# Optimization experiments

Hardware: AMD Instinct MI355X
Metric: run time of the kernel (lower is better)

The kernel has to match this reference:

```python
import jax, jax.numpy as jnp
import numpy as np

N = 100000
HEADS = 8
HID = 8  # per-head channels of gat1
NUM_CLASSES = 40
NUM_FEATURES = 256
NEG_SLOPE = 0.2


def gat_conv(x, src, dst, W, att_src, att_dst, bias, heads, out_ch, concat):
    # x: [N, F_in]; src/dst: [E] (self-loops already included)
    n = x.shape[0]
    h = (x @ W).reshape(n, heads, out_ch)                      # [N, H, C]
    a_src = jnp.sum(h * att_src, axis=-1)                      # [N, H]
    a_dst = jnp.sum(h * att_dst, axis=-1)                      # [N, H]
    e = jax.nn.leaky_relu(a_src[src] + a_dst[dst], NEG_SLOPE)  # [E, H]
    # segment softmax over edges grouped by destination node
    e_max = jax.ops.segment_max(e, dst, num_segments=n)        # [N, H]
    w = jnp.exp(e - e_max[dst])                                # [E, H]
    denom = jax.ops.segment_sum(w, dst, num_segments=n)        # [N, H]
    alpha = w / (denom[dst] + 1e-16)                           # [E, H]
    out = jax.ops.segment_sum(h[src] * alpha[:, :, None], dst, num_segments=n)  # [N, H, C]
    out = out.reshape(n, heads * out_ch) if concat else out.mean(axis=1)
    return out + bias


def setup_inputs() -> dict:
    key = jax.random.key(0)
    ks = jax.random.split(key, 12)
    x = jax.random.normal(ks[0], (N, NUM_FEATURES), dtype=jnp.float32)
    edge_index = jax.random.randint(ks[1], (2, 3200000), 0, N, dtype=jnp.int64)
    g1 = (2.0 / (NUM_FEATURES + HEADS * HID)) ** 0.5
    g2 = (2.0 / (HEADS * HID + NUM_CLASSES)) ** 0.5
    return {
        "x": x,
        "edge_index": edge_index,
        "W1": jax.random.normal(ks[2], (NUM_FEATURES, HEADS * HID), dtype=jnp.float32) * g1,
        "att_src1": jax.random.normal(ks[3], (HEADS, HID), dtype=jnp.float32) * g1,
        "att_dst1": jax.random.normal(ks[4], (HEADS, HID), dtype=jnp.float32) * g1,
        "b1": jnp.zeros((HEADS * HID,), dtype=jnp.float32),
        "W2": jax.random.normal(ks[5], (HEADS * HID, NUM_CLASSES), dtype=jnp.float32) * g2,
        "att_src2": jax.random.normal(ks[6], (1, NUM_CLASSES), dtype=jnp.float32) * g2,
        "att_dst2": jax.random.normal(ks[7], (1, NUM_CLASSES), dtype=jnp.float32) * g2,
        "b2": jnp.zeros((NUM_CLASSES,), dtype=jnp.float32),
    }


def reference(x, edge_index, W1, att_src1, att_dst1, b1, W2, att_src2, att_dst2, b2):
    n = x.shape[0]
    # add self loops (PyG GATConv default) -> every segment is non-empty
    loops = jnp.arange(n, dtype=edge_index.dtype)
    src = jnp.concatenate([edge_index[0], loops])
    dst = jnp.concatenate([edge_index[1], loops])
    # dropout is identity in eval mode
    h = gat_conv(x, src, dst, W1, att_src1, att_dst1, b1, HEADS, HID, concat=True)
    h = jax.nn.elu(h)
    out = gat_conv(h, src, dst, W2, att_src2, att_dst2, b2, 1, NUM_CLASSES, concat=False)
    return jax.nn.log_softmax(out, axis=1)
```

## Files before the change

### kernel.cpp

```cpp
#include <hip/hip_runtime.h>
#include <hip/hip_bf16.h>
#include <cstdint>
#include <cstddef>

#define NNODES 100000
#define NEDGES 3200000
#define NTOT   3300000
#define FIN    256
#define HH     64
#define NH     8
#define C2     40
#define NEG    0.2f

#define CHUNK  8192
#define NBLK   403
#define NBKT   391

typedef __hip_bfloat16 bf16;
typedef __attribute__((ext_vector_type(8))) short short8;
typedef __attribute__((ext_vector_type(4))) float f32x4;


__global__ __launch_bounds__(256) void k_bhist(const int* __restrict__ ei, int* __restrict__ bhist) {
    __shared__ int h[NBKT];
    int t = threadIdx.x;
    for (int b = t; b < NBKT; b += 256) h[b] = 0;
    __syncthreads();
    int i0 = blockIdx.x * CHUNK;
    int i1 = i0 + CHUNK; if (i1 > NTOT) i1 = NTOT;
    for (int i = i0 + t; i < i1; i += 256) {
        int d = (i < NEDGES) ? ei[NEDGES + i] : (i - NEDGES);
        atomicAdd(&h[d >> 8], 1);
    }
    __syncthreads();
    for (int b = t; b < NBKT; b += 256) bhist[b * NBLK + blockIdx.x] = h[b];
}

__global__ __launch_bounds__(512) void k_bscan(int* __restrict__ bhist, int* __restrict__ bktTot) {
    __shared__ int sm[512];
    int t = threadIdx.x, b = blockIdx.x;
    int v = (t < NBLK) ? bhist[b * NBLK + t] : 0;
    sm[t] = v;
    __syncthreads();
    for (int off = 1; off < 512; off <<= 1) {
        int u = (t >= off) ? sm[t - off] : 0;
        __syncthreads();
        sm[t] += u;
        __syncthreads();
    }
    if (t < NBLK) bhist[b * NBLK + t] = sm[t] - v;
    if (t == NBLK - 1) bktTot[b] = sm[t];
}

__global__ __launch_bounds__(512) void k_base(const int* __restrict__ bktTot, int* __restrict__ bktBase,
                                              int* __restrict__ rowptr) {
    __shared__ int sm[512];
    int t = threadIdx.x;
    int v = (t < NBKT) ? bktTot[t] : 0;
    sm[t] = v;
    __syncthreads();
    for (int off = 1; off < 512; off <<= 1) {
        int u = (t >= off) ? sm[t - off] : 0;
        __syncthreads();
        sm[t] += u;
        __syncthreads();
    }
    if (t < NBKT) bktBase[t] = sm[t] - v;
    if (t == NBKT - 1) bktBase[NBKT] = sm[t];
    if (t == 0) rowptr[NNODES] = NTOT;
}

__global__ __launch_bounds__(256) void k_scat1(const int* __restrict__ ei, const int* __restrict__ bhist,
                                               const int* __restrict__ bktBase, unsigned int* __restrict__ pb) {
    __shared__ int cur[NBKT];
    int t = threadIdx.x, blk = blockIdx.x;
    for (int b = t; b < NBKT; b += 256) cur[b] = bktBase[b] + bhist[b * NBLK + blk];
    __syncthreads();
    int i0 = blk * CHUNK;
    int i1 = i0 + CHUNK; if (i1 > NTOT) i1 = NTOT;
    for (int i = i0 + t; i < i1; i += 256) {
        int s, d;
        if (i < NEDGES) { s = ei[i]; d = ei[NEDGES + i]; }
        else            { s = d = i - NEDGES; }
        int p = atomicAdd(&cur[d >> 8], 1);
        pb[p] = ((unsigned)s << 8) | (unsigned)(d & 255);
    }
}

__global__ __launch_bounds__(256) void k_bucket(const unsigned int* __restrict__ pb,
                                                const int* __restrict__ bktBase,
                                                int* __restrict__ rowptr, int* __restrict__ esrc) {
    __shared__ int dcnt[256];
    __shared__ int sm[256];
    __shared__ int cur[256];
    int t = threadIdx.x, b = blockIdx.x;
    int base = bktBase[b], cnt = bktBase[b + 1] - base;
    dcnt[t] = 0;
    __syncthreads();
    for (int i = t; i < cnt; i += 256) atomicAdd(&dcnt[pb[base + i] & 255], 1);
    __syncthreads();
    int v = dcnt[t];
    sm[t] = v;
    __syncthreads();
    for (int off = 1; off < 256; off <<= 1) {
        int u = (t >= off) ? sm[t - off] : 0;
        __syncthreads();
        sm[t] += u;
        __syncthreads();
    }
    int ex = sm[t] - v;
    int n = (b << 8) + t;
    if (n < NNODES) rowptr[n] = base + ex;
    cur[t] = base + ex;
    __syncthreads();
    for (int i = t; i < cnt; i += 256) {
        unsigned int e = pb[base + i];
        int p = atomicAdd(&cur[e & 255], 1);
        esrc[p] = (int)(e >> 8);
    }
}


__global__ __launch_bounds__(256) void k_wcvt(const float* __restrict__ W, bf16* __restrict__ Wf) {
    int idx = blockIdx.x * 256 + threadIdx.x;
    int j = idx & 7, slot = idx >> 3;
    int l = slot & 63, sf = slot >> 6;
    int s = sf >> 2, f = sf & 3;
    int k = s * 32 + (l >> 4) * 8 + j;
    int c = 16 * f + (l & 15);
    Wf[idx] = __float2bfloat16(W[k * HH + c]);
}

__global__ __launch_bounds__(256) void k_gemm1(const float* __restrict__ x, const bf16* __restrict__ Wf,
                                               const float* __restrict__ asw, const float* __restrict__ adw,
                                               bf16* __restrict__ h1b, float* __restrict__ as,
                                               float* __restrict__ ad) {
    __shared__ short xs[64][256];
    int t = threadIdx.x;
    int n0 = blockIdx.x * 64;
    {
        int r = t >> 2, cq = t & 3;
        int n = n0 + r; if (n >= NNODES) n = NNODES - 1;
        const float4* xr = (const float4*)(x + (size_t)n * FIN + cq * 64);
        int sw = r & 7;
#pragma unroll
        for (int u = 0; u < 8; ++u) {
            float4 p0 = xr[2 * u], p1 = xr[2 * u + 1];
            float tmp[8] = {p0.x, p0.y, p0.z, p0.w, p1.x, p1.y, p1.z, p1.w};
            short8 v;
#pragma unroll
            for (int e = 0; e < 8; ++e) {
                bf16 b = __float2bfloat16(tmp[e]);
                v[e] = *reinterpret_cast<short*>(&b);
            }
            int kb = cq * 8 + u;
            *(short8*)&xs[r][(kb ^ sw) << 3] = v;
        }
    }
    __syncthreads();
    int l = t & 63, wv = t >> 6;
    int rbase = wv * 16;
    int lr = l & 15, g = l >> 4;
    f32x4 acc[4] = {{0.f,0.f,0.f,0.f},{0.f,0.f,0.f,0.f},{0.f,0.f,0.f,0.f},{0.f,0.f,0.f,0.f}};
    const short8* wfp = (const short8*)Wf;
#pragma unroll 2
    for (int s = 0; s < 8; ++s) {
        short8 a = *(const short8*)&xs[rbase + lr][((s * 4 + g) ^ (lr & 7)) << 3];
#pragma unroll
        for (int f = 0; f < 4; ++f) {
            short8 b = wfp[(s * 4 + f) * 64 + l];
            acc[f] = __builtin_amdgcn_mfma_f32_16x16x32_bf16(a, b, acc[f], 0, 0, 0);
        }
    }
    float awf[4], dwf[4];
#pragma unroll
    for (int f = 0; f < 4; ++f) { awf[f] = asw[16 * f + lr]; dwf[f] = adw[16 * f + lr]; }
    float svv[4][4], dvv[4][4];
#pragma unroll
    for (int f = 0; f < 4; ++f) {
#pragma unroll
        for (int j = 0; j < 4; ++j) {
            float val = acc[f][j];
            int n = n0 + rbase + g * 4 + j;
            if (n < NNODES) h1b[(size_t)n * HH + 16 * f + lr] = __float2bfloat16(val);
            float sv = val * awf[f], dv = val * dwf[f];
            sv += __shfl_xor(sv, 1); sv += __shfl_xor(sv, 2); sv += __shfl_xor(sv, 4);
            dv += __shfl_xor(dv, 1); dv += __shfl_xor(dv, 2); dv += __shfl_xor(dv, 4);
            svv[f][j] = sv; dvv[f][j] = dv;
        }
    }
    if ((l & 7) == 0) {
        int hb = (l >> 3) & 1;
#pragma unroll
        for (int f = 0; f < 4; ++f) {
            int h = 2 * f + hb;
#pragma unroll
            for (int j = 0; j < 4; ++j) {
                int n = n0 + rbase + g * 4 + j;
                if (n < NNODES) { as[n * NH + h] = svv[f][j]; ad[n * NH + h] = dvv[f][j]; }
            }
        }
    }
}

__global__ __launch_bounds__(256) void k_aggr1(const bf16* __restrict__ h1b, const float* __restrict__ as,
                                               const float* __restrict__ ad, const int* __restrict__ rowptr,
                                               const int* __restrict__ esrc, const float* __restrict__ b1,
                                               float* __restrict__ hmid) {
    __shared__ float wlds[4][64];
    int wv = threadIdx.x >> 6, t = threadIdx.x & 63;
    int n = blockIdx.x * 4 + wv;
    int ih = t & 7;
    int ie = t >> 3;
    int h  = t >> 3;
    float adh = ad[n * NH + ih];
    int beg = __builtin_amdgcn_readfirstlane(rowptr[n]);
    int end = __builtin_amdgcn_readfirstlane(rowptr[n + 1]);
    float acc = 0.f, den_e = 0.f;
    int idx0 = beg + ie; if (idx0 >= end) idx0 = end - 1;
    int s_t = esrc[idx0];
    float a_t = as[s_t * NH + ih];
    for (int j0 = beg; j0 < end; j0 += 8) {
        int m = end - j0; if (m > 8) m = 8;
        float e = a_t + adh;
        e = (e > 0.f) ? e : NEG * e;
        float w_t = (ie < m) ? __expf(e) : 0.f;
        den_e += w_t;
        wlds[wv][t] = w_t;
        __builtin_amdgcn_wave_barrier();
        if (j0 + 8 < end) {
            int idx = j0 + 8 + ie; if (idx >= end) idx = end - 1;
            s_t = esrc[idx];
            a_t = as[s_t * NH + ih];
        }
        const int* ep = esrc + j0;
        if (m == 8) {
#pragma unroll
            for (int k = 0; k < 8; ++k) {
                int sk = __builtin_amdgcn_readfirstlane(ep[k]);
                float vk = __bfloat162float(h1b[(size_t)sk * HH + t]);
                acc = fmaf(wlds[wv][k * 8 + h], vk, acc);
            }
        } else {
            for (int k = 0; k < m; ++k) {
                int sk = __builtin_amdgcn_readfirstlane(ep[k]);
                float vk = __bfloat162float(h1b[(size_t)sk * HH + t]);
                acc = fmaf(wlds[wv][k * 8 + h], vk, acc);
            }
        }
        __builtin_amdgcn_wave_barrier();
    }
    den_e += __shfl_xor(den_e, 8);
    den_e += __shfl_xor(den_e, 16);
    den_e += __shfl_xor(den_e, 32);
    float den = __shfl(den_e, h);
    float o = acc / (den + 1e-16f) + b1[t];
    hmid[(size_t)n * HH + t] = (o > 0.f) ? o : expm1f(o);
}


__global__ __launch_bounds__(256) void k_gemm2(const float* __restrict__ hmid, const float* __restrict__ W2,
                                               const float* __restrict__ as2w, const float* __restrict__ ad2w,
                                               bf16* __restrict__ h2b, float* __restrict__ as2,
                                               float* __restrict__ ad2) {
    __shared__ float w2s[64 * C2];
    __shared__ float hrow[4][64];
    int t = threadIdx.x;
    for (int i = t; i < 64 * C2; i += 256) w2s[i] = W2[i];
    __syncthreads();
    int wv = t >> 6, ln = t & 63;
    int n = blockIdx.x * 4 + wv;
    hrow[wv][ln] = hmid[(size_t)n * HH + ln];
    __syncthreads();
    float acc = 0.f;
    if (ln < C2) {
#pragma unroll 8
        for (int k = 0; k < 64; ++k) acc = fmaf(hrow[wv][k], w2s[k * C2 + ln], acc);
    }
    float sv = 0.f, dv = 0.f;
    if (ln < C2) {
        h2b[(size_t)n * C2 + ln] = __float2bfloat16(acc);
        sv = acc * as2w[ln];
        dv = acc * ad2w[ln];
    }
#pragma unroll
    for (int off = 32; off > 0; off >>= 1) {
        sv += __shfl_xor(sv, off);
        dv += __shfl_xor(dv, off);
    }
    if (ln == 0) { as2[n] = sv; ad2[n] = dv; }
}

__global__ __launch_bounds__(256) void k_aggr2(const bf16* __restrict__ h2b, const float* __restrict__ as2,
                                               const float* __restrict__ ad2, const int* __restrict__ rowptr,
                                               const int* __restrict__ esrc, const float* __restrict__ b2,
                                               float* __restrict__ out) {
    int wv = threadIdx.x >> 6, t = threadIdx.x & 63;
    int n = blockIdx.x * 4 + wv;
    float adn = ad2[n];
    int beg = __builtin_amdgcn_readfirstlane(rowptr[n]);
    int end = __builtin_amdgcn_readfirstlane(rowptr[n + 1]);
    bool act = (t < C2);
    int tc = act ? t : 0;
    float acc = 0.f, den_p = 0.f;
    for (int j0 = beg; j0 < end; j0 += 64) {
        int m = end - j0; if (m > 64) m = 64;
        int idx = j0 + t; if (idx >= end) idx = end - 1;
        int s_t = esrc[idx];
        float e = as2[s_t] + adn;
        e = (e > 0.f) ? e : NEG * e;
        float w_t = (t < m) ? __expf(e) : 0.f;
        den_p += w_t;
        const int* ep = esrc + j0;
        int k = 0;
        for (; k + 8 <= m; k += 8) {
#pragma unroll
            for (int u = 0; u < 8; ++u) {
                int sk = __builtin_amdgcn_readfirstlane(ep[k + u]);
                float wk = __shfl(w_t, k + u);
                acc = fmaf(wk, __bfloat162float(h2b[(size_t)sk * C2 + tc]), acc);
            }
        }
        for (; k < m; ++k) {
            int sk = __builtin_amdgcn_readfirstlane(ep[k]);
            float wk = __shfl(w_t, k);
            acc = fmaf(wk, __bfloat162float(h2b[(size_t)sk * C2 + tc]), acc);
        }
    }
    float den = den_p;
#pragma unroll
    for (int off = 32; off > 0; off >>= 1) den += __shfl_xor(den, off);
    float o = act ? (acc / (den + 1e-16f) + b2[t]) : -1e30f;
    float mx = o;
#pragma unroll
    for (int off = 32; off > 0; off >>= 1) mx = fmaxf(mx, __shfl_xor(mx, off));
    float ex = act ? __expf(o - mx) : 0.f;
    float sm = ex;
#pragma unroll
    for (int off = 32; off > 0; off >>= 1) sm += __shfl_xor(sm, off);
    if (act) out[(size_t)n * C2 + t] = o - mx - logf(sm);
}


extern "C" void kernel_launch(void* const* d_in, const int* in_sizes, int n_in,
                              void* d_out, int out_size, void* d_ws, size_t ws_size,
                              hipStream_t stream) {
    const float* x    = (const float*)d_in[0];
    const int*   ei   = (const int*)d_in[1];
    const float* W1   = (const float*)d_in[2];
    const float* as1w = (const float*)d_in[3];
    const float* ad1w = (const float*)d_in[4];
    const float* b1   = (const float*)d_in[5];
    const float* W2   = (const float*)d_in[6];
    const float* as2w = (const float*)d_in[7];
    const float* ad2w = (const float*)d_in[8];
    const float* b2   = (const float*)d_in[9];
    float* out = (float*)d_out;

    char* ws = (char*)d_ws;
    bf16*  h1b     = (bf16*) (ws + 0);
    float* as1     = (float*)(ws + 12800000);
    float* ad1     = (float*)(ws + 16000000);
    float* hmid    = (float*)(ws + 19200000);
    unsigned int* pb = (unsigned int*)(ws + 19200000);
    bf16*  h2b     = (bf16*) (ws + 44800000);
    int*   bhist   = (int*)  (ws + 44800000);
    float* as2     = (float*)(ws + 52800000);
    int*   bktBase = (int*)  (ws + 52800000);
    float* ad2     = (float*)(ws + 53200000);
    int*   bktTot  = (int*)  (ws + 53200000);
    int*   rowp    = (int*)  (ws + 53600000);
    int*   esrc    = (int*)  (ws + 54000256);
    bf16*  Wf      = (bf16*) (ws + 67201024);

    k_bhist <<<NBLK, 256, 0, stream>>>(ei, bhist);
    k_bscan <<<NBKT, 512, 0, stream>>>(bhist, bktTot);
    k_base  <<<1,    512, 0, stream>>>(bktTot, bktBase, rowp);
    k_scat1 <<<NBLK, 256, 0, stream>>>(ei, bhist, bktBase, pb);
    k_bucket<<<NBKT, 256, 0, stream>>>(pb, bktBase, rowp, esrc);
    k_wcvt  <<<64, 256, 0, stream>>>(W1, Wf);
    k_gemm1 <<<(NNODES + 63) / 64, 256, 0, stream>>>(x, Wf, as1w, ad1w, h1b, as1, ad1);
    k_aggr1 <<<NNODES / 4, 256, 0, stream>>>(h1b, as1, ad1, rowp, esrc, b1, hmid);
    k_gemm2 <<<NNODES / 4, 256, 0, stream>>>(hmid, W2, as2w, ad2w, h2b, as2, ad2);
    k_aggr2 <<<NNODES / 4, 256, 0, stream>>>(h2b, as2, ad2, rowp, esrc, b2, out);
}
```

Measured before the change: 349.1 us.

## Split layer-1 features into head-pair quarters and aggregate per quarter

Layer-1 features and source attention scores are stored in four head-pair planes, so each plane is a compact 3.2 MB (features) or 0.8 MB (scores) array. The layer-1 aggregation now launches one block per quarter of four nodes, so each gather touches only that quarter's plane. It also processes 64 edges per wave iteration, with 4 edges gathered in parallel across lane groups. This aims to improve cache locality of the random source-node gathers and edge-level parallelism, at the cost of reading the edge list and row pointers four times and more blocks.

```diff
diff --git a/kernel.cpp b/kernel.cpp
--- a/kernel.cpp
+++ b/kernel.cpp
@@ -133,7 +133,7 @@
 
 __global__ __launch_bounds__(256) void k_gemm1(const float* __restrict__ x, const bf16* __restrict__ Wf,
                                                const float* __restrict__ asw, const float* __restrict__ adw,
-                                               bf16* __restrict__ h1b, float* __restrict__ as,
+                                               bf16* __restrict__ h1q, float* __restrict__ as1q,
                                                float* __restrict__ ad) {
     __shared__ short xs[64][256];
     int t = threadIdx.x;
@@ -182,7 +182,7 @@
         for (int j = 0; j < 4; ++j) {
             float val = acc[f][j];
             int n = n0 + rbase + g * 4 + j;
-            if (n < NNODES) h1b[(size_t)n * HH + 16 * f + lr] = __float2bfloat16(val);
+            if (n < NNODES) h1q[(size_t)f * (NNODES * 16) + (size_t)n * 16 + lr] = __float2bfloat16(val);
             float sv = val * awf[f], dv = val * dwf[f];
             sv += __shfl_xor(sv, 1); sv += __shfl_xor(sv, 2); sv += __shfl_xor(sv, 4);
             dv += __shfl_xor(dv, 1); dv += __shfl_xor(dv, 2); dv += __shfl_xor(dv, 4);
@@ -193,69 +193,68 @@
         int hb = (l >> 3) & 1;
 #pragma unroll
         for (int f = 0; f < 4; ++f) {
-            int h = 2 * f + hb;
 #pragma unroll
             for (int j = 0; j < 4; ++j) {
                 int n = n0 + rbase + g * 4 + j;
-                if (n < NNODES) { as[n * NH + h] = svv[f][j]; ad[n * NH + h] = dvv[f][j]; }
+                if (n < NNODES) {
+                    as1q[(size_t)f * (NNODES * 2) + n * 2 + hb] = svv[f][j];
+                    ad[n * NH + 2 * f + hb] = dvv[f][j];
+                }
             }
         }
     }
 }
 
-__global__ __launch_bounds__(256) void k_aggr1(const bf16* __restrict__ h1b, const float* __restrict__ as,
+__global__ __launch_bounds__(256) void k_aggr1(const bf16* __restrict__ h1q, const float* __restrict__ as1q,
                                                const float* __restrict__ ad, const int* __restrict__ rowptr,
                                                const int* __restrict__ esrc, const float* __restrict__ b1,
                                                float* __restrict__ hmid) {
-    __shared__ float wlds[4][64];
+    __shared__ float wlds[4][128];
+    __shared__ int   slds[4][64];
+    int bid = blockIdx.x;
+    int q = bid & 3, g = bid >> 2;
     int wv = threadIdx.x >> 6, t = threadIdx.x & 63;
-    int n = blockIdx.x * 4 + wv;
-    int ih = t & 7;
-    int ie = t >> 3;
-    int h  = t >> 3;
-    float adh = ad[n * NH + ih];
+    int n = g * 4 + wv;
+    const bf16*  hq = h1q  + (size_t)q * (NNODES * 16);
+    const float* aq = as1q + (size_t)q * (NNODES * 2);
+    float adh0 = ad[n * NH + 2 * q];
+    float adh1 = ad[n * NH + 2 * q + 1];
     int beg = __builtin_amdgcn_readfirstlane(rowptr[n]);
     int end = __builtin_amdgcn_readfirstlane(rowptr[n + 1]);
-    float acc = 0.f, den_e = 0.f;
-    int idx0 = beg + ie; if (idx0 >= end) idx0 = end - 1;
-    int s_t = esrc[idx0];
-    float a_t = as[s_t * NH + ih];
-    for (int j0 = beg; j0 < end; j0 += 8) {
-        int m = end - j0; if (m > 8) m = 8;
-        float e = a_t + adh;
-        e = (e > 0.f) ? e : NEG * e;
-        float w_t = (ie < m) ? __expf(e) : 0.f;
-        den_e += w_t;
-        wlds[wv][t] = w_t;
+    int e4 = t >> 4, c = t & 15, hb = (t >> 3) & 1;
+    float acc = 0.f, den = 0.f;
+    for (int j0 = beg; j0 < end; j0 += 64) {
+        int m = end - j0; if (m > 64) m = 64;
+        int idx = j0 + t; if (idx >= end) idx = end - 1;
+        int s_t = esrc[idx];
+        float2 a2 = *(const float2*)&aq[s_t * 2];
+        float e0 = a2.x + adh0; e0 = (e0 > 0.f) ? e0 : NEG * e0;
+        float e1 = a2.y + adh1; e1 = (e1 > 0.f) ? e1 : NEG * e1;
+        bool vld = (t < m);
+        float w0 = vld ? __expf(e0) : 0.f;
+        float w1 = vld ? __expf(e1) : 0.f;
+        slds[wv][t] = s_t;
+        wlds[wv][t * 2]     = w0;
+        wlds[wv][t * 2 + 1] = w1;
         __builtin_amdgcn_wave_barrier();
-        if (j0 + 8 < end) {
-            int idx = j0 + 8 + ie; if (idx >= end) idx = end - 1;
-            s_t = esrc[idx];
-            a_t = as[s_t * NH + ih];
-        }
-        const int* ep = esrc + j0;
-        if (m == 8) {
-#pragma unroll
-            for (int k = 0; k < 8; ++k) {
-                int sk = __builtin_amdgcn_readfirstlane(ep[k]);
-                float vk = __bfloat162float(h1b[(size_t)sk * HH + t]);
-                acc = fmaf(wlds[wv][k * 8 + h], vk, acc);
-            }
-        } else {
-            for (int k = 0; k < m; ++k) {
-                int sk = __builtin_amdgcn_readfirstlane(ep[k]);
-                float vk = __bfloat162float(h1b[(size_t)sk * HH + t]);
-                acc = fmaf(wlds[wv][k * 8 + h], vk, acc);
-            }
+        int iters = (m + 3) >> 2;
+#pragma unroll 4
+        for (int kk = 0; kk < iters; ++kk) {
+            int eb = kk * 4 + e4;
+            int se = slds[wv][eb];
+            float wk = wlds[wv][eb * 2 + hb];
+            float v = __bfloat162float(hq[(size_t)se * 16 + c]);
+            den += wk;
+            acc = fmaf(wk, v, acc);
         }
         __builtin_amdgcn_wave_barrier();
     }
-    den_e += __shfl_xor(den_e, 8);
-    den_e += __shfl_xor(den_e, 16);
-    den_e += __shfl_xor(den_e, 32);
-    float den = __shfl(den_e, h);
-    float o = acc / (den + 1e-16f) + b1[t];
-    hmid[(size_t)n * HH + t] = (o > 0.f) ? o : expm1f(o);
+    acc += __shfl_xor(acc, 16); acc += __shfl_xor(acc, 32);
+    den += __shfl_xor(den, 16); den += __shfl_xor(den, 32);
+    if (t < 16) {
+        float o = acc / (den + 1e-16f) + b1[q * 16 + t];
+        hmid[(size_t)n * HH + q * 16 + t] = (o > 0.f) ? o : expm1f(o);
+    }
 }
 
 
@@ -358,8 +357,8 @@
     float* out = (float*)d_out;
 
     char* ws = (char*)d_ws;
-    bf16*  h1b     = (bf16*) (ws + 0);
-    float* as1     = (float*)(ws + 12800000);
+    bf16*  h1q     = (bf16*) (ws + 0);
+    float* as1q    = (float*)(ws + 12800000);
     float* ad1     = (float*)(ws + 16000000);
     float* hmid    = (float*)(ws + 19200000);
     unsigned int* pb = (unsigned int*)(ws + 19200000);
@@ -379,8 +378,8 @@
     k_scat1 <<<NBLK, 256, 0, stream>>>(ei, bhist, bktBase, pb);
     k_bucket<<<NBKT, 256, 0, stream>>>(pb, bktBase, rowp, esrc);
     k_wcvt  <<<64, 256, 0, stream>>>(W1, Wf);
-    k_gemm1 <<<(NNODES + 63) / 64, 256, 0, stream>>>(x, Wf, as1w, ad1w, h1b, as1, ad1);
-    k_aggr1 <<<NNODES / 4, 256, 0, stream>>>(h1b, as1, ad1, rowp, esrc, b1, hmid);
+    k_gemm1 <<<(NNODES + 63) / 64, 256, 0, stream>>>(x, Wf, as1w, ad1w, h1q, as1q, ad1);
+    k_aggr1 <<<NNODES, 256, 0, stream>>>(h1q, as1q, ad1, rowp, esrc, b1, hmid);
     k_gemm2 <<<NNODES / 4, 256, 0, stream>>>(hmid, W2, as2w, ad2w, h2b, as2, ad2);
     k_aggr2 <<<NNODES / 4, 256, 0, stream>>>(h2b, as2, ad2, rowp, esrc, b2, out);
 }
```

Result: slower. 422.1 us (+20.9%).
